# Kernel tuning notes

Hardware: AMD Instinct MI355X
Metric: run time of the kernel (lower is better)

## Reference

```python
import jax, jax.numpy as jnp
import numpy as np

N_QUBITS = 4
DIM = 2 ** N_QUBITS  # 16
B = 262144
N_FEATURES = 64


def _apply_ry(state, theta, q):
    # state: (B, 16) complex64; theta: scalar or (B,) angle; RY on wire q (wire 0 = MSB)
    b = state.shape[0]
    L, R = 2 ** q, 2 ** (N_QUBITS - 1 - q)
    s = state.reshape(b, L, 2, R)
    theta = jnp.broadcast_to(jnp.asarray(theta, jnp.float32), (b,))
    c = jnp.cos(theta * 0.5)[:, None, None]
    sn = jnp.sin(theta * 0.5)[:, None, None]
    s0, s1 = s[:, :, 0], s[:, :, 1]
    n0 = c * s0 - sn * s1
    n1 = sn * s0 + c * s1
    return jnp.stack([n0, n1], axis=2).reshape(b, DIM)


def _apply_rz(state, theta, q):
    # RZ(theta) = diag(exp(-i theta/2), exp(+i theta/2)) on wire q
    b = state.shape[0]
    L, R = 2 ** q, 2 ** (N_QUBITS - 1 - q)
    s = state.reshape(b, L, 2, R)
    theta = jnp.broadcast_to(jnp.asarray(theta, jnp.float32), (b,))
    p = jnp.exp(-0.5j * theta)[:, None, None].astype(state.dtype)
    n0 = s[:, :, 0] * p
    n1 = s[:, :, 1] * jnp.conj(p)
    return jnp.stack([n0, n1], axis=2).reshape(b, DIM)


def _cnot(state, c):
    # CNOT with control wire c, target wire c+1 (adjacent, as in the circuit)
    b = state.shape[0]
    L, R = 2 ** c, 2 ** (N_QUBITS - 2 - c)
    s = state.reshape(b, L, 2, 2, R)
    s1 = jnp.flip(s[:, :, 1], axis=2)  # flip target when control=1
    return jnp.stack([s[:, :, 0], s1], axis=2).reshape(b, DIM)


def _simulate(angles, w):
    # angles: (B, 4) input RY rotations; w: (8, 2) trainable gate angles
    b = angles.shape[0]
    state = jnp.zeros((b, DIM), jnp.complex64).at[:, 0].set(1.0)
    for q in range(N_QUBITS):
        state = _apply_ry(state, angles[:, q], q)
    for q in range(N_QUBITS):
        state = _apply_rz(state, w[q, 0], q)
        state = _apply_ry(state, w[q, 1], q)
    for q in range(N_QUBITS - 1):
        state = _cnot(state, q)
    for q in range(N_QUBITS):
        state = _apply_rz(state, w[q + N_QUBITS, 0], q)
        state = _apply_ry(state, w[q + N_QUBITS, 1], q)
    probs = (state.real ** 2 + state.imag ** 2).reshape((b,) + (2,) * N_QUBITS)
    outs = []
    for q in range(N_QUBITS):
        axes = tuple(a for a in range(1, N_QUBITS + 1) if a != q + 1)
        p = probs.sum(axis=axes)  # (B, 2)
        outs.append(p[:, 0] - p[:, 1])  # <Z_q>
    return jnp.stack(outs, axis=1).astype(jnp.float32)


def setup_inputs() -> dict:
    key = jax.random.key(0)
    k1, k2, k3 = jax.random.split(key, 3)
    x = jax.random.normal(k1, (B, N_FEATURES), jnp.float32)
    fm_w = jax.random.normal(k2, (N_QUBITS, N_FEATURES), jnp.float32) / jnp.sqrt(N_FEATURES)
    fm_b = jnp.zeros((N_QUBITS,), jnp.float32)
    # TorchLayer default init: uniform(0, 2*pi)
    q_weights = jax.random.uniform(k3, (2 * N_QUBITS, 2), jnp.float32, 0.0, 2.0 * np.pi)
    return {"x": x, "fm_w": fm_w, "fm_b": fm_b, "q_weights": q_weights}


def reference(x, fm_w, fm_b, q_weights):
    angles = x @ fm_w.T + fm_b  # feature_map Linear(n_features -> n_qubits)
    return _simulate(angles, q_weights)  # (B, n_qubits) Pauli-Z expectations
```

## Files before the change

kernel.cpp:

```cpp
#include <hip/hip_runtime.h>

#define NQ 4
#define DIM 16
#define TPB 256


template <int BIT>
__device__ __forceinline__ void rz_gate(float* re, float* im, float cz, float sz) {
#pragma unroll
    for (int k = 0; k < DIM; ++k) {
        const float ss = (k & BIT) ? -sz : sz;
        const float nr = re[k] * cz + im[k] * ss;
        const float ni = im[k] * cz - re[k] * ss;
        re[k] = nr; im[k] = ni;
    }
}

template <int BIT>
__device__ __forceinline__ void ry_gate(float* re, float* im, float cy, float sy) {
#pragma unroll
    for (int k = 0; k < DIM; ++k) {
        if (!(k & BIT)) {
            const int k1 = k | BIT;
            const float r0 = re[k], i0 = im[k], r1 = re[k1], i1 = im[k1];
            re[k]  = cy * r0 - sy * r1;  im[k]  = cy * i0 - sy * i1;
            re[k1] = sy * r0 + cy * r1;  im[k1] = sy * i0 + cy * i1;
        }
    }
}

template <int CB, int TB>
__device__ __forceinline__ void cnot(float* re, float* im) {
    float tr[DIM], ti[DIM];
#pragma unroll
    for (int k = 0; k < DIM; ++k) {
        const int ks = (k & CB) ? (k ^ TB) : k;
        tr[k] = re[ks]; ti[k] = im[ks];
    }
#pragma unroll
    for (int k = 0; k < DIM; ++k) { re[k] = tr[k]; im[k] = ti[k]; }
}

__global__ __launch_bounds__(TPB, 4) void qnn_fused(
    const float* __restrict__ x, const float* __restrict__ fm_w,
    const float* __restrict__ fm_b, const float* __restrict__ w,
    float* __restrict__ out, int B) {
    const long long b = (long long)blockIdx.x * TPB + threadIdx.x;
    if (b >= B) return;

    float acc[NQ];
#pragma unroll
    for (int q = 0; q < NQ; ++q) acc[q] = fm_b[q];

    const float4* __restrict__ x4 = (const float4*)(x + b * 64);
    const float4* __restrict__ w4 = (const float4*)fm_w;
#pragma unroll
    for (int t = 0; t < 16; ++t) {
        const float4 xv = x4[t];
#pragma unroll
        for (int q = 0; q < NQ; ++q) {
            const float4 wv = w4[q * 16 + t];
            acc[q] += xv.x * wv.x + xv.y * wv.y + xv.z * wv.z + xv.w * wv.w;
        }
    }

    float c[NQ], s[NQ];
#pragma unroll
    for (int q = 0; q < NQ; ++q) __sincosf(0.5f * acc[q], &s[q], &c[q]);

    float p01[4], p23[4];
#pragma unroll
    for (int u = 0; u < 4; ++u) {
        p01[u] = ((u & 2) ? s[0] : c[0]) * ((u & 1) ? s[1] : c[1]);
        p23[u] = ((u & 2) ? s[2] : c[2]) * ((u & 1) ? s[3] : c[3]);
    }
    float st[DIM];
#pragma unroll
    for (int i = 0; i < DIM; ++i) st[i] = p01[i >> 2] * p23[i & 3];

    float re[DIM], im[DIM];

    {
        float sz, cz; __sincosf(0.5f * w[0], &sz, &cz);
#pragma unroll
        for (int k = 0; k < DIM; ++k) {
            re[k] = st[k] * cz;
            im[k] = (k & 8) ? st[k] * sz : -(st[k] * sz);
        }
    }
    {
        float sy, cy; __sincosf(0.5f * w[1], &sy, &cy);
        ry_gate<8>(re, im, cy, sy);
    }
    {
        float sz, cz; __sincosf(0.5f * w[2], &sz, &cz);
        rz_gate<4>(re, im, cz, sz);
        float sy, cy; __sincosf(0.5f * w[3], &sy, &cy);
        ry_gate<4>(re, im, cy, sy);
    }
    {
        float sz, cz; __sincosf(0.5f * w[4], &sz, &cz);
        rz_gate<2>(re, im, cz, sz);
        float sy, cy; __sincosf(0.5f * w[5], &sy, &cy);
        ry_gate<2>(re, im, cy, sy);
    }
    {
        float sz, cz; __sincosf(0.5f * w[6], &sz, &cz);
        rz_gate<1>(re, im, cz, sz);
        float sy, cy; __sincosf(0.5f * w[7], &sy, &cy);
        ry_gate<1>(re, im, cy, sy);
    }

    cnot<8, 4>(re, im);
    cnot<4, 2>(re, im);
    cnot<2, 1>(re, im);

    {
        float sz, cz; __sincosf(0.5f * w[8], &sz, &cz);
        rz_gate<8>(re, im, cz, sz);
        float sy, cy; __sincosf(0.5f * w[9], &sy, &cy);
        ry_gate<8>(re, im, cy, sy);
    }
    {
        float sz, cz; __sincosf(0.5f * w[10], &sz, &cz);
        rz_gate<4>(re, im, cz, sz);
        float sy, cy; __sincosf(0.5f * w[11], &sy, &cy);
        ry_gate<4>(re, im, cy, sy);
    }
    {
        float sz, cz; __sincosf(0.5f * w[12], &sz, &cz);
        rz_gate<2>(re, im, cz, sz);
        float sy, cy; __sincosf(0.5f * w[13], &sy, &cy);
        ry_gate<2>(re, im, cy, sy);
    }
    {
        float sz, cz; __sincosf(0.5f * w[14], &sz, &cz);
        rz_gate<1>(re, im, cz, sz);
        float sy, cy; __sincosf(0.5f * w[15], &sy, &cy);
        ry_gate<1>(re, im, cy, sy);
    }

    float o0 = 0.f, o1 = 0.f, o2 = 0.f, o3 = 0.f;
#pragma unroll
    for (int k = 0; k < DIM; ++k) {
        const float pk = re[k] * re[k] + im[k] * im[k];
        o0 += (k & 8) ? -pk : pk;
        o1 += (k & 4) ? -pk : pk;
        o2 += (k & 2) ? -pk : pk;
        o3 += (k & 1) ? -pk : pk;
    }

    *(float4*)(out + b * 4) = make_float4(o0, o1, o2, o3);
}

extern "C" void kernel_launch(void* const* d_in, const int* in_sizes, int n_in,
                              void* d_out, int out_size, void* d_ws, size_t ws_size,
                              hipStream_t stream) {
    const float* x    = (const float*)d_in[0];
    const float* fm_w = (const float*)d_in[1];
    const float* fm_b = (const float*)d_in[2];
    const float* qw   = (const float*)d_in[3];
    float* out = (float*)d_out;

    const int B = in_sizes[0] / 64;

    qnn_fused<<<(B + TPB - 1) / TPB, TPB, 0, stream>>>(x, fm_w, fm_b, qw, out, B);
}
```

Measured before the change: 24.86 us.

## Coalesce feature-map loads by splitting each row across eight lanes with shuffles

The 64-wide dot product for each batch row is now split across 8 cooperating lanes. Each lane loads a contiguous 32-byte slice and the partial sums are reduced with xor shuffles. This replaces the per-thread strided 256-byte row reads with coalesced wavefront loads of contiguous rows. The trade-off is extra shuffle instructions and registers for the cached weight slices.

```diff
diff --git a/kernel.cpp b/kernel.cpp
--- a/kernel.cpp
+++ b/kernel.cpp
@@ -41,32 +41,58 @@
     for (int k = 0; k < DIM; ++k) { re[k] = tr[k]; im[k] = ti[k]; }
 }
 
+__device__ __forceinline__ float dot44(const float4 a, const float4 w) {
+    return a.x * w.x + a.y * w.y + a.z * w.z + a.w * w.w;
+}
+
 __global__ __launch_bounds__(TPB, 4) void qnn_fused(
     const float* __restrict__ x, const float* __restrict__ fm_w,
     const float* __restrict__ fm_b, const float* __restrict__ w,
     float* __restrict__ out, int B) {
-    const long long b = (long long)blockIdx.x * TPB + threadIdx.x;
-    if (b >= B) return;
+    const int tid = threadIdx.x;
+    const int lane = tid & 63;
+    const int g = lane >> 3;
+    const int o = lane & 7;
+    const long long wbase = (long long)blockIdx.x * TPB + (tid & ~63);
 
-    float acc[NQ];
+    const float4* __restrict__ w4 = (const float4*)fm_w;
+    float4 wf[8];
 #pragma unroll
-    for (int q = 0; q < NQ; ++q) acc[q] = fm_b[q];
+    for (int q = 0; q < NQ; ++q) {
+        wf[q * 2 + 0] = w4[q * 16 + o * 2 + 0];
+        wf[q * 2 + 1] = w4[q * 16 + o * 2 + 1];
+    }
 
-    const float4* __restrict__ x4 = (const float4*)(x + b * 64);
-    const float4* __restrict__ w4 = (const float4*)fm_w;
+    float ang[NQ] = {0.f, 0.f, 0.f, 0.f};
 #pragma unroll
-    for (int t = 0; t < 16; ++t) {
-        const float4 xv = x4[t];
+    for (int i = 0; i < 8; ++i) {
+        const long long r = wbase + g * 8 + i;
+        float4 xa = make_float4(0.f, 0.f, 0.f, 0.f), xb = xa;
+        if (r < B) {
+            const float4* __restrict__ xp = (const float4*)(x + r * 64) + o * 2;
+            xa = xp[0]; xb = xp[1];
+        }
+        float d[NQ];
 #pragma unroll
-        for (int q = 0; q < NQ; ++q) {
-            const float4 wv = w4[q * 16 + t];
-            acc[q] += xv.x * wv.x + xv.y * wv.y + xv.z * wv.z + xv.w * wv.w;
+        for (int q = 0; q < NQ; ++q)
+            d[q] = dot44(xa, wf[q * 2]) + dot44(xb, wf[q * 2 + 1]);
+#pragma unroll
+        for (int m = 1; m <= 4; m <<= 1) {
+#pragma unroll
+            for (int q = 0; q < NQ; ++q) d[q] += __shfl_xor(d[q], m);
+        }
+        if (o == i) {
+#pragma unroll
+            for (int q = 0; q < NQ; ++q) ang[q] = d[q] + fm_b[q];
         }
     }
 
+    const long long b = wbase + g * 8 + o;
+    if (b >= B) return;
+
     float c[NQ], s[NQ];
 #pragma unroll
-    for (int q = 0; q < NQ; ++q) __sincosf(0.5f * acc[q], &s[q], &c[q]);
+    for (int q = 0; q < NQ; ++q) __sincosf(0.5f * ang[q], &s[q], &c[q]);
 
     float p01[4], p23[4];
 #pragma unroll
@@ -79,7 +105,6 @@
     for (int i = 0; i < DIM; ++i) st[i] = p01[i >> 2] * p23[i & 3];
 
     float re[DIM], im[DIM];
-
     {
         float sz, cz; __sincosf(0.5f * w[0], &sz, &cz);
 #pragma unroll
```

Measured after the change: 24.78 us. Within noise of the previous version (-0.3%).
